# Optimization experiments

Measured on AMD Instinct MI355X. Metric: run time of the kernel, lower is better.

The kernel has to match this reference:

```python
import jax, jax.numpy as jnp
import numpy as np

B, N, C, L, E = 8, 8192, 256, 4, 131072  # graphs, nodes/graph, channels (in=hidden=out), layers, edges/graph


def setup_inputs() -> dict:
    key = jax.random.key(0)
    ks = jax.random.split(key, 9)
    batch_node_tsr = jax.random.normal(ks[0], (B, N, C), jnp.float32)
    edge_index = jax.random.randint(ks[1], (B, 2, E), 0, N, jnp.int32)
    batch_last_node_idx_list = jnp.arange(1, B + 1, dtype=jnp.int32) * N - 1
    s1 = 1.0 / np.sqrt(C)
    s2 = 1.0 / np.sqrt(2 * C)
    # Base GraphConv layers: out = x @ Wr.T + sum_nbr(x) @ Wn.T + b  (all CxC since in=hidden=out)
    base_Wr = jax.random.uniform(ks[2], (L, C, C), jnp.float32, -s1, s1)
    base_Wn = jax.random.uniform(ks[3], (L, C, C), jnp.float32, -s1, s1)
    base_b = jax.random.uniform(ks[4], (L, C), jnp.float32, -s1, s1)
    # Adapter GraphConv layers take concatenated (2C) input
    adapt_Wr = jax.random.uniform(ks[5], (L, C, 2 * C), jnp.float32, -s2, s2)
    adapt_Wn = jax.random.uniform(ks[6], (L, C, 2 * C), jnp.float32, -s2, s2)
    adapt_b = jax.random.uniform(ks[7], (L, C), jnp.float32, -s2, s2)
    return dict(batch_node_tsr=batch_node_tsr, base_Wr=base_Wr, base_Wn=base_Wn,
                base_b=base_b, adapt_Wr=adapt_Wr, adapt_Wn=adapt_Wn, adapt_b=adapt_b,
                edge_index=edge_index, batch_last_node_idx_list=batch_last_node_idx_list)


def reference(batch_node_tsr, base_Wr, base_Wn, base_b, adapt_Wr, adapt_Wn, adapt_b,
              edge_index, batch_last_node_idx_list):
    # Batch graphs PyG-style: offset per-graph node indices into one big graph
    offsets = (jnp.arange(B, dtype=edge_index.dtype) * N)[:, None]  # [B,1]
    src = (edge_index[:, 0, :] + offsets).reshape(-1)  # [B*E]
    dst = (edge_index[:, 1, :] + offsets).reshape(-1)  # [B*E]
    x = batch_node_tsr.reshape(B * N, C)

    def gconv(h, Wr, Wn, b):
        # GraphConv: root transform + sum-aggregated neighbor transform
        agg = jax.ops.segment_sum(h[src], dst, num_segments=B * N)
        return h @ Wr.T + agg @ Wn.T + b

    # Base encoder pass, keeping all latent embeds
    lat = [x]
    for i in range(L):
        lat.append(jax.nn.relu(gconv(lat[-1], base_Wr[i], base_Wn[i], base_b[i])))
    base_batch_embed = lat[-1].reshape(B, N, C)

    # Adapter pass: concat(base_latent[i+1], curr) -> adapter GraphConv -> relu
    curr = x
    for i in range(L):
        curr = jax.nn.relu(gconv(jnp.concatenate([lat[i + 1], curr], axis=-1),
                                 adapt_Wr[i], adapt_Wn[i], adapt_b[i]))
    adapter_batch_embed = curr.reshape(B, N, C)
    return base_batch_embed, adapter_batch_embed
```

## Files before the change

kernel.cpp:

```cpp
#include <hip/hip_runtime.h>

#define B_ 8
#define N_ 8192
#define C_ 256
#define L_ 4
#define E_ 131072
#define BN_ 65536
#define EDGES_ 1048576
#define NKEY_ (BN_ * 4)

typedef __attribute__((ext_vector_type(8))) short short8;
typedef __attribute__((ext_vector_type(4))) float f32x4;

__device__ __forceinline__ unsigned short f2bf(float f){
  unsigned int u = __builtin_bit_cast(unsigned int, f);
  u += 0x7fffu + ((u >> 16) & 1u);
  return (unsigned short)(u >> 16);
}
__device__ __forceinline__ float bf2f(unsigned short h){
  unsigned int u = ((unsigned int)h) << 16;
  return __builtin_bit_cast(float, u);
}

__launch_bounds__(256)
__global__ void cvt_bf16_k(const float* __restrict__ in, unsigned short* __restrict__ out, int n4){
  int t = blockIdx.x * 256 + threadIdx.x;
  if (t >= n4) return;
  float4 v = ((const float4*)in)[t];
  ushort4 o;
  o.x = f2bf(v.x); o.y = f2bf(v.y); o.z = f2bf(v.z); o.w = f2bf(v.w);
  ((ushort4*)out)[t] = o;
}

__launch_bounds__(256)
__global__ void hist_k(const int* __restrict__ ei, int* __restrict__ cnt){
  int t = blockIdx.x * 256 + threadIdx.x;
  int b = t >> 17, e = t & (E_ - 1);
  int src = ei[b * (2 * E_) + e];
  int dst = ei[b * (2 * E_) + E_ + e];
  int key = (((b << 13) + dst) << 2) | (src >> 11);
  atomicAdd(&cnt[key], 1);
}

__launch_bounds__(256)
__global__ void scan_k(const int* __restrict__ cnt, int* __restrict__ row_ptr, int* __restrict__ cursor){
  __shared__ int lsum[256];
  int t = threadIdx.x;
  const int CH = NKEY_ / 256;
  int base = t * CH;
  int s = 0;
  const int4* c4 = (const int4*)(cnt + base);
  for (int i = 0; i < CH / 4; ++i){ int4 v = c4[i]; s += v.x + v.y + v.z + v.w; }
  lsum[t] = s;
  __syncthreads();
  for (int d = 1; d < 256; d <<= 1){
    int v = (t >= d) ? lsum[t - d] : 0;
    __syncthreads();
    lsum[t] += v;
    __syncthreads();
  }
  int off = lsum[t] - s;
  for (int i = 0; i < CH; ++i){
    row_ptr[base + i] = off;
    cursor[base + i]  = off;
    off += cnt[base + i];
  }
  if (t == 255) row_ptr[NKEY_] = off;
}

__launch_bounds__(256)
__global__ void scat_k(const int* __restrict__ ei, int* __restrict__ cursor, int* __restrict__ col){
  int t = blockIdx.x * 256 + threadIdx.x;
  int b = t >> 17, e = t & (E_ - 1);
  int src = ei[b * (2 * E_) + e];
  int dst = ei[b * (2 * E_) + E_ + e];
  int key = (((b << 13) + dst) << 2) | (src >> 11);
  int pos = atomicAdd(&cursor[key], 1);
  col[pos] = (b << 13) + src;
}

__launch_bounds__(256)
__global__ void agg_k(const unsigned short* __restrict__ feat, const int* __restrict__ row_ptr,
                      const int* __restrict__ col, unsigned short* __restrict__ out){
  int w = threadIdx.x >> 6, lane = threadIdx.x & 63;
  int g = blockIdx.x & 7, sblk = blockIdx.x >> 3;
  int node = (g << 13) + (sblk << 2) + w;
  int beg = row_ptr[node << 2], end = row_ptr[(node << 2) + 4];
  int ch = lane << 2;
  float a0=0,a1=0,a2=0,a3=0;
  int e = beg;
  for (; e + 4 <= end; e += 4){
    int s0 = col[e], s1 = col[e+1], s2 = col[e+2], s3 = col[e+3];
    ushort4 v0 = *(const ushort4*)(feat + ((size_t)s0 << 8) + ch);
    ushort4 v1 = *(const ushort4*)(feat + ((size_t)s1 << 8) + ch);
    ushort4 v2 = *(const ushort4*)(feat + ((size_t)s2 << 8) + ch);
    ushort4 v3 = *(const ushort4*)(feat + ((size_t)s3 << 8) + ch);
    a0 += (bf2f(v0.x) + bf2f(v1.x)) + (bf2f(v2.x) + bf2f(v3.x));
    a1 += (bf2f(v0.y) + bf2f(v1.y)) + (bf2f(v2.y) + bf2f(v3.y));
    a2 += (bf2f(v0.z) + bf2f(v1.z)) + (bf2f(v2.z) + bf2f(v3.z));
    a3 += (bf2f(v0.w) + bf2f(v1.w)) + (bf2f(v2.w) + bf2f(v3.w));
  }
  for (; e < end; ++e){
    int s0 = col[e];
    ushort4 v0 = *(const ushort4*)(feat + ((size_t)s0 << 8) + ch);
    a0 += bf2f(v0.x); a1 += bf2f(v0.y); a2 += bf2f(v0.z); a3 += bf2f(v0.w);
  }
  ushort4 o;
  o.x = f2bf(a0); o.y = f2bf(a1); o.z = f2bf(a2); o.w = f2bf(a3);
  *(ushort4*)(out + ((size_t)node << 8) + ch) = o;
}

__launch_bounds__(256)
__global__ void agg2_k(const unsigned short* __restrict__ fA, const unsigned short* __restrict__ fB,
                       const int* __restrict__ row_ptr, const int* __restrict__ col,
                       unsigned short* __restrict__ oA, unsigned short* __restrict__ oB){
  int w = threadIdx.x >> 6, lane = threadIdx.x & 63;
  int g = blockIdx.x & 7, sblk = blockIdx.x >> 3;
  int node = (g << 13) + (sblk << 2) + w;
  int beg = row_ptr[node << 2], end = row_ptr[(node << 2) + 4];
  int ch = lane << 2;
  float a0=0,a1=0,a2=0,a3=0, c0=0,c1=0,c2=0,c3=0;
  int e = beg;
  for (; e + 4 <= end; e += 4){
    int s0 = col[e], s1 = col[e+1], s2 = col[e+2], s3 = col[e+3];
    ushort4 va0 = *(const ushort4*)(fA + ((size_t)s0 << 8) + ch);
    ushort4 va1 = *(const ushort4*)(fA + ((size_t)s1 << 8) + ch);
    ushort4 va2 = *(const ushort4*)(fA + ((size_t)s2 << 8) + ch);
    ushort4 va3 = *(const ushort4*)(fA + ((size_t)s3 << 8) + ch);
    ushort4 vb0 = *(const ushort4*)(fB + ((size_t)s0 << 8) + ch);
    ushort4 vb1 = *(const ushort4*)(fB + ((size_t)s1 << 8) + ch);
    ushort4 vb2 = *(const ushort4*)(fB + ((size_t)s2 << 8) + ch);
    ushort4 vb3 = *(const ushort4*)(fB + ((size_t)s3 << 8) + ch);
    a0 += (bf2f(va0.x) + bf2f(va1.x)) + (bf2f(va2.x) + bf2f(va3.x));
    a1 += (bf2f(va0.y) + bf2f(va1.y)) + (bf2f(va2.y) + bf2f(va3.y));
    a2 += (bf2f(va0.z) + bf2f(va1.z)) + (bf2f(va2.z) + bf2f(va3.z));
    a3 += (bf2f(va0.w) + bf2f(va1.w)) + (bf2f(va2.w) + bf2f(va3.w));
    c0 += (bf2f(vb0.x) + bf2f(vb1.x)) + (bf2f(vb2.x) + bf2f(vb3.x));
    c1 += (bf2f(vb0.y) + bf2f(vb1.y)) + (bf2f(vb2.y) + bf2f(vb3.y));
    c2 += (bf2f(vb0.z) + bf2f(vb1.z)) + (bf2f(vb2.z) + bf2f(vb3.z));
    c3 += (bf2f(vb0.w) + bf2f(vb1.w)) + (bf2f(vb2.w) + bf2f(vb3.w));
  }
  for (; e < end; ++e){
    int s0 = col[e];
    ushort4 va0 = *(const ushort4*)(fA + ((size_t)s0 << 8) + ch);
    ushort4 vb0 = *(const ushort4*)(fB + ((size_t)s0 << 8) + ch);
    a0 += bf2f(va0.x); a1 += bf2f(va0.y); a2 += bf2f(va0.z); a3 += bf2f(va0.w);
    c0 += bf2f(vb0.x); c1 += bf2f(vb0.y); c2 += bf2f(vb0.z); c3 += bf2f(vb0.w);
  }
  ushort4 oa, ob;
  oa.x = f2bf(a0); oa.y = f2bf(a1); oa.z = f2bf(a2); oa.w = f2bf(a3);
  ob.x = f2bf(c0); ob.y = f2bf(c1); ob.z = f2bf(c2); ob.w = f2bf(c3);
  *(ushort4*)(oA + ((size_t)node << 8) + ch) = oa;
  *(ushort4*)(oB + ((size_t)node << 8) + ch) = ob;
}

#define GLDS16(gp, lp) __builtin_amdgcn_global_load_lds( \
    (const __attribute__((address_space(1))) void*)(gp), \
    (__attribute__((address_space(3))) void*)(lp), 16, 0, 0)

template<int P>
__launch_bounds__(256)
__global__ void gemm_k(const unsigned short* __restrict__ A0, const unsigned short* __restrict__ A1,
                       const unsigned short* __restrict__ A2, const unsigned short* __restrict__ A3,
                       const unsigned short* __restrict__ W0, const unsigned short* __restrict__ W1,
                       const unsigned short* __restrict__ W2, const unsigned short* __restrict__ W3,
                       int ldw, const float* __restrict__ bias,
                       unsigned short* __restrict__ outb, float* __restrict__ outf){
  __shared__ unsigned short lds_u[24576];
  const unsigned short* As[4] = {A0, A1, A2, A3};
  const unsigned short* Ws[4] = {W0, W1, W2, W3};
  const int m0 = blockIdx.x << 7;
  const int t = threadIdx.x, lane = t & 63;
  const int w = t >> 6;
  const int lrow = lane & 15, kg = lane >> 4;
  f32x4 acc[2][16] = {};
  int cur = 0;

#pragma unroll
  for (int p = 0; p < P; ++p){
    const unsigned short* A = As[p] + (size_t)m0 * C_;
    const unsigned short* W = Ws[p];
    {
      unsigned short* a_t = lds_u + cur * 12288;
      unsigned short* b_t = a_t + 4096;
#pragma unroll
      for (int c = t; c < 512; c += 256){
        int row = c >> 2, seg = c & 3;
        GLDS16(A + row * C_  + seg * 8, &a_t[c * 8]);
      }
#pragma unroll
      for (int c = t; c < 1024; c += 256){
        int row = c >> 2, seg = c & 3;
        GLDS16(W + row * ldw + seg * 8, &b_t[c * 8]);
      }
      asm volatile("s_waitcnt vmcnt(0)" ::: "memory");
      __builtin_amdgcn_s_barrier();
    }
    for (int ks = 0; ks < 8; ++ks){
      if (ks < 7){
        int k0 = (ks + 1) << 5;
        unsigned short* a_t = lds_u + (cur ^ 1) * 12288;
        unsigned short* b_t = a_t + 4096;
#pragma unroll
        for (int c = t; c < 512; c += 256){
          int row = c >> 2, seg = c & 3;
          GLDS16(A + row * C_  + k0 + seg * 8, &a_t[c * 8]);
        }
#pragma unroll
        for (int c = t; c < 1024; c += 256){
          int row = c >> 2, seg = c & 3;
          GLDS16(W + row * ldw + k0 + seg * 8, &b_t[c * 8]);
        }
      }
      {
        const unsigned short* a_t = lds_u + cur * 12288;
        const unsigned short* b_t = a_t + 4096;
        short8 af[2];
#pragma unroll
        for (int m = 0; m < 2; ++m)
          af[m] = *(const short8*)&a_t[((w << 5) + (m << 4) + lrow) * 32 + (kg << 3)];
#pragma unroll
        for (int h = 0; h < 2; ++h){
          short8 bfr[8];
#pragma unroll
          for (int n2 = 0; n2 < 8; ++n2)
            bfr[n2] = *(const short8*)&b_t[((h << 7) + (n2 << 4) + lrow) * 32 + (kg << 3)];
#pragma unroll
          for (int m = 0; m < 2; ++m)
#pragma unroll
            for (int n2 = 0; n2 < 8; ++n2)
              acc[m][(h << 3) + n2] =
                  __builtin_amdgcn_mfma_f32_16x16x32_bf16(af[m], bfr[n2], acc[m][(h << 3) + n2], 0, 0, 0);
        }
      }
      asm volatile("s_waitcnt vmcnt(0)" ::: "memory");
      __builtin_amdgcn_s_barrier();
      cur ^= 1;
    }
  }
  float bv[16];
#pragma unroll
  for (int n = 0; n < 16; ++n) bv[n] = bias[(n << 4) + lrow];
  unsigned short* ep  = lds_u + (w << 11);
  float*          epf = (float*)(&lds_u[8192]) + (w << 11);
#pragma unroll
  for (int m = 0; m < 2; ++m){
    const int gr = m0 + (w << 5) + (m << 4);
    if (outf){
#pragma unroll
      for (int h = 0; h < 2; ++h){
#pragma unroll
        for (int n2 = 0; n2 < 8; ++n2){
          int n = (h << 3) + n2;
#pragma unroll
          for (int j = 0; j < 4; ++j){
            float v = acc[m][n][j] + bv[n];
            v = v > 0.f ? v : 0.f;
            epf[((kg << 2) + j) * 128 + (n2 << 4) + lrow] = v;
          }
        }
#pragma unroll
        for (int k = 0; k < 8; ++k){
          int r = (lane >> 5) + (k << 1);
          float4 v = *(const float4*)&epf[r * 128 + (lane & 31) * 4];
          *(float4*)&outf[(size_t)(gr + r) * C_ + (h << 7) + (lane & 31) * 4] = v;
        }
      }
    }
    if (outb){
#pragma unroll
      for (int h = 0; h < 2; ++h){
#pragma unroll
        for (int n2 = 0; n2 < 8; ++n2){
          int n = (h << 3) + n2;
#pragma unroll
          for (int j = 0; j < 4; ++j){
            float v = acc[m][n][j] + bv[n];
            v = v > 0.f ? v : 0.f;
            ep[((kg << 2) + j) * 128 + (n2 << 4) + lrow] = f2bf(v);
          }
        }
#pragma unroll
        for (int k = 0; k < 4; ++k){
          int r = (lane >> 4) + (k << 2);
          short8 v = *(const short8*)&ep[r * 128 + (lane & 15) * 8];
          *(short8*)&outb[(size_t)(gr + r) * C_ + (h << 7) + (lane & 15) * 8] = v;
        }
      }
    }
  }
}

extern "C" void kernel_launch(void* const* d_in, const int* in_sizes, int n_in,
                              void* d_out, int out_size, void* d_ws, size_t ws_size,
                              hipStream_t stream){
  const float* x_f   = (const float*)d_in[0];
  const float* bWr_f = (const float*)d_in[1];
  const float* bWn_f = (const float*)d_in[2];
  const float* bB    = (const float*)d_in[3];
  const float* aWr_f = (const float*)d_in[4];
  const float* aWn_f = (const float*)d_in[5];
  const float* aB    = (const float*)d_in[6];
  const int*   ei    = (const int*)d_in[7];
  float* out = (float*)d_out;
  (void)in_sizes; (void)n_in; (void)out_size; (void)ws_size;

  char* p = (char*)d_ws;
  const size_t BUF = (size_t)BN_ * C_ * sizeof(unsigned short);
  auto alloc = [&](size_t bytes){ void* r = (void*)p; p += (bytes + 255) & ~(size_t)255; return r; };
  unsigned short* xb   = (unsigned short*)alloc(BUF);
  unsigned short* latA = (unsigned short*)alloc(BUF);
  unsigned short* latB = (unsigned short*)alloc(BUF);
  unsigned short* curA = (unsigned short*)alloc(BUF);
  unsigned short* curB = (unsigned short*)alloc(BUF);
  unsigned short* agg0 = (unsigned short*)alloc(BUF);
  unsigned short* agg1 = (unsigned short*)alloc(BUF);
  unsigned short* wbR  = (unsigned short*)alloc((size_t)L_ * C_ * C_ * 2);
  unsigned short* wbN  = (unsigned short*)alloc((size_t)L_ * C_ * C_ * 2);
  unsigned short* waR  = (unsigned short*)alloc((size_t)L_ * C_ * 2 * C_ * 2);
  unsigned short* waN  = (unsigned short*)alloc((size_t)L_ * C_ * 2 * C_ * 2);
  int* cnt     = (int*)alloc((size_t)NKEY_ * 4);
  int* row_ptr = (int*)alloc((size_t)(NKEY_ + 1) * 4);
  int* cursor  = (int*)alloc((size_t)NKEY_ * 4);
  int* colx    = (int*)alloc((size_t)EDGES_ * 4);

  cvt_bf16_k<<<BN_ * C_ / 4 / 256, 256, 0, stream>>>(x_f, xb, BN_ * C_ / 4);
  cvt_bf16_k<<<L_ * C_ * C_ / 4 / 256, 256, 0, stream>>>(bWr_f, wbR, L_ * C_ * C_ / 4);
  cvt_bf16_k<<<L_ * C_ * C_ / 4 / 256, 256, 0, stream>>>(bWn_f, wbN, L_ * C_ * C_ / 4);
  cvt_bf16_k<<<L_ * C_ * 2 * C_ / 4 / 256, 256, 0, stream>>>(aWr_f, waR, L_ * C_ * 2 * C_ / 4);
  cvt_bf16_k<<<L_ * C_ * 2 * C_ / 4 / 256, 256, 0, stream>>>(aWn_f, waN, L_ * C_ * 2 * C_ / 4);

  hipMemsetAsync(cnt, 0, (size_t)NKEY_ * 4, stream);
  hist_k<<<EDGES_ / 256, 256, 0, stream>>>(ei, cnt);
  scan_k<<<1, 256, 0, stream>>>(cnt, row_ptr, cursor);
  scat_k<<<EDGES_ / 256, 256, 0, stream>>>(ei, cursor, colx);

  const int AGG_GRID  = BN_ / 4;
  const int GEMM_GRID = BN_ / 128;

  const size_t WB = (size_t)C_ * C_;
  const size_t WA = (size_t)C_ * 2 * C_;

  agg_k<<<AGG_GRID, 256, 0, stream>>>(xb, row_ptr, colx, agg0);
  gemm_k<2><<<GEMM_GRID, 256, 0, stream>>>(xb, agg0, nullptr, nullptr,
      wbR, wbN, nullptr, nullptr, C_, bB, latA, nullptr);
  agg_k<<<AGG_GRID, 256, 0, stream>>>(latA, row_ptr, colx, agg1);
  gemm_k<2><<<GEMM_GRID, 256, 0, stream>>>(latA, agg1, nullptr, nullptr,
      wbR + WB, wbN + WB, nullptr, nullptr, C_, bB + 256, latB, nullptr);
  gemm_k<4><<<GEMM_GRID, 256, 0, stream>>>(latA, xb, agg1, agg0,
      waR, waR + 256, waN, waN + 256, 2 * C_, aB, curA, nullptr);
  agg2_k<<<AGG_GRID, 256, 0, stream>>>(latB, curA, row_ptr, colx, agg1, agg0);
  gemm_k<2><<<GEMM_GRID, 256, 0, stream>>>(latB, agg1, nullptr, nullptr,
      wbR + 2 * WB, wbN + 2 * WB, nullptr, nullptr, C_, bB + 512, latA, nullptr);
  gemm_k<4><<<GEMM_GRID, 256, 0, stream>>>(latB, curA, agg1, agg0,
      waR + WA, waR + WA + 256, waN + WA, waN + WA + 256, 2 * C_, aB + 256, curB, nullptr);
  agg2_k<<<AGG_GRID, 256, 0, stream>>>(latA, curB, row_ptr, colx, agg1, agg0);
  gemm_k<2><<<GEMM_GRID, 256, 0, stream>>>(latA, agg1, nullptr, nullptr,
      wbR + 3 * WB, wbN + 3 * WB, nullptr, nullptr, C_, bB + 768, latB, out);
  gemm_k<4><<<GEMM_GRID, 256, 0, stream>>>(latA, curB, agg1, agg0,
      waR + 2 * WA, waR + 2 * WA + 256, waN + 2 * WA, waN + 2 * WA + 256, 2 * C_, aB + 512, curA, nullptr);
  agg2_k<<<AGG_GRID, 256, 0, stream>>>(latB, curA, row_ptr, colx, agg1, agg0);
  gemm_k<4><<<GEMM_GRID, 256, 0, stream>>>(latB, curA, agg1, agg0,
      waR + 3 * WA, waR + 3 * WA + 256, waN + 3 * WA, waN + 3 * WA + 256, 2 * C_, aB + 768,
      nullptr, out + (size_t)BN_ * C_);
}
```

Baseline: 1.234 ms.

## Replace single-block CSR prefix scan with three-phase multi-block scan

The single-block exclusive scan over the 262144 bucket counts is split into three kernels: per-block reductions, a scan of the block sums, and a per-block local scan that writes row_ptr and cursor with vectorized stores. This removes a serial, poorly parallel scan where one workgroup processed all keys. It adds two extra kernel launches and small scratch buffers, and it sets the final row pointer to the known total edge count.

```diff
diff --git a/kernel.cpp b/kernel.cpp
--- a/kernel.cpp
+++ b/kernel.cpp
@@ -43,29 +43,59 @@
 }
 
 __launch_bounds__(256)
-__global__ void scan_k(const int* __restrict__ cnt, int* __restrict__ row_ptr, int* __restrict__ cursor){
-  __shared__ int lsum[256];
+__global__ void scanA_k(const int* __restrict__ cnt, int* __restrict__ bsum){
+  __shared__ int ls[256];
+  int b = blockIdx.x, t = threadIdx.x;
+  int4 v = *(const int4*)(cnt + b * 1024 + t * 4);
+  int s = v.x + v.y + v.z + v.w;
+  ls[t] = s;
+  __syncthreads();
+  for (int d = 128; d > 0; d >>= 1){
+    if (t < d) ls[t] += ls[t + d];
+    __syncthreads();
+  }
+  if (t == 0) bsum[b] = ls[0];
+}
+__launch_bounds__(256)
+__global__ void scanB_k(const int* __restrict__ bsum, int* __restrict__ boff){
+  __shared__ int ls[256];
   int t = threadIdx.x;
-  const int CH = NKEY_ / 256;
-  int base = t * CH;
-  int s = 0;
-  const int4* c4 = (const int4*)(cnt + base);
-  for (int i = 0; i < CH / 4; ++i){ int4 v = c4[i]; s += v.x + v.y + v.z + v.w; }
-  lsum[t] = s;
+  int v = bsum[t];
+  ls[t] = v;
   __syncthreads();
   for (int d = 1; d < 256; d <<= 1){
-    int v = (t >= d) ? lsum[t - d] : 0;
+    int x = (t >= d) ? ls[t - d] : 0;
     __syncthreads();
-    lsum[t] += v;
+    ls[t] += x;
     __syncthreads();
   }
-  int off = lsum[t] - s;
-  for (int i = 0; i < CH; ++i){
-    row_ptr[base + i] = off;
-    cursor[base + i]  = off;
-    off += cnt[base + i];
-  }
-  if (t == 255) row_ptr[NKEY_] = off;
+  boff[t] = ls[t] - v;
+}
+__launch_bounds__(256)
+__global__ void scanC_k(const int* __restrict__ cnt, const int* __restrict__ boff,
+                        int* __restrict__ row_ptr, int* __restrict__ cursor){
+  __shared__ int ls[256];
+  int b = blockIdx.x, t = threadIdx.x;
+  int base = b * 1024 + t * 4;
+  int4 v = *(const int4*)(cnt + base);
+  int s = v.x + v.y + v.z + v.w;
+  ls[t] = s;
+  __syncthreads();
+  for (int d = 1; d < 256; d <<= 1){
+    int x = (t >= d) ? ls[t - d] : 0;
+    __syncthreads();
+    ls[t] += x;
+    __syncthreads();
+  }
+  int off = boff[b] + ls[t] - s;
+  int4 rp;
+  rp.x = off;
+  rp.y = off + v.x;
+  rp.z = rp.y + v.y;
+  rp.w = rp.z + v.z;
+  *(int4*)(row_ptr + base) = rp;
+  *(int4*)(cursor + base) = rp;
+  if (b == 255 && t == 255) row_ptr[NKEY_] = EDGES_;
 }
 
 __launch_bounds__(256)
@@ -323,6 +353,8 @@
   int* row_ptr = (int*)alloc((size_t)(NKEY_ + 1) * 4);
   int* cursor  = (int*)alloc((size_t)NKEY_ * 4);
   int* colx    = (int*)alloc((size_t)EDGES_ * 4);
+  int* bsum    = (int*)alloc(256 * 4);
+  int* boff    = (int*)alloc(256 * 4);
 
   cvt_bf16_k<<<BN_ * C_ / 4 / 256, 256, 0, stream>>>(x_f, xb, BN_ * C_ / 4);
   cvt_bf16_k<<<L_ * C_ * C_ / 4 / 256, 256, 0, stream>>>(bWr_f, wbR, L_ * C_ * C_ / 4);
@@ -332,7 +364,9 @@
 
   hipMemsetAsync(cnt, 0, (size_t)NKEY_ * 4, stream);
   hist_k<<<EDGES_ / 256, 256, 0, stream>>>(ei, cnt);
-  scan_k<<<1, 256, 0, stream>>>(cnt, row_ptr, cursor);
+  scanA_k<<<256, 256, 0, stream>>>(cnt, bsum);
+  scanB_k<<<1, 256, 0, stream>>>(bsum, boff);
+  scanC_k<<<256, 256, 0, stream>>>(cnt, boff, row_ptr, cursor);
   scat_k<<<EDGES_ / 256, 256, 0, stream>>>(ei, cursor, colx);
 
   const int AGG_GRID  = BN_ / 4;
```

Result: faster. 1.103 ms (-10.6%).
